# Performance work log

Hardware: AMD Instinct MI355X
Metric: run time of the kernel (lower is better)

The kernel has to match this reference:

```python
import jax, jax.numpy as jnp
import numpy as np

TOP_K = 2
B, S, H, I, E = 1, 2048, 1024, 4096, 8


def setup_inputs() -> dict:
    key = jax.random.key(0)
    k1, k2, k3, k4 = jax.random.split(key, 4)
    x = jax.random.normal(k1, (B, S, H), dtype=jnp.float32)
    gate_w = jax.random.normal(k2, (E, H), dtype=jnp.float32)
    w1 = jax.random.normal(k3, (E, I, H), dtype=jnp.float32)
    w2 = jax.random.normal(k4, (E, H, I), dtype=jnp.float32)
    return {"x": x, "gate_w": gate_w, "w1": w1, "w2": w2}


def reference(x, gate_w, w1, w2):
    b, s, h = x.shape
    xf = x.reshape(-1, h)                      # [T, H]
    T = xf.shape[0]
    logits = xf @ gate_w.T                     # [T, E]
    probs = jax.nn.softmax(logits, axis=-1)
    wts, idx = jax.lax.top_k(probs, TOP_K)     # [T, k]
    wts = wts / jnp.sum(wts, axis=-1, keepdims=True)
    # combine[t, e] = routing weight of expert e for token t (0 if not selected)
    combine = jnp.zeros((T, w1.shape[0]), dtype=x.dtype)
    combine = combine.at[jnp.arange(T)[:, None], idx].add(wts)
    # dense dispatch: every expert processes every token, masked/weighted by combine
    hid = jax.nn.silu(jnp.einsum('th,eih->tei', xf, w1))   # [T, E, I]
    y = jnp.einsum('tei,ehi->teh', hid, w2)                # [T, E, H]
    out = jnp.einsum('teh,te->th', y, combine)             # [T, H]
    return out.reshape(b, s, h)
```

## Files before the change

kernel.cpp:

```cpp
#include <hip/hip_runtime.h>
#include <stdint.h>

#define TT 2048
#define HH 1024
#define II 4096
#define EE 8
#define KS 4
#define KSPAN (II / KS)

typedef __attribute__((ext_vector_type(4))) float floatx4;
typedef __attribute__((ext_vector_type(8))) __bf16 bf16x8;

__device__ __forceinline__ unsigned short f2bf(float f) {
  union { float f; unsigned u; } v; v.f = f;
  return (unsigned short)((v.u + 0x7FFFu + ((v.u >> 16) & 1u)) >> 16);
}

__device__ __forceinline__ void async_ld16(const void* g, void* l) {
  __builtin_amdgcn_global_load_lds(
      (__attribute__((address_space(1))) void*)g,
      (__attribute__((address_space(3))) void*)l, 16, 0, 0);
}

#define CFENCE asm volatile("" ::: "memory")
#define WAIT_VM(n) asm volatile("s_waitcnt vmcnt(" #n ")" ::: "memory")
#define WAIT_LGKM0 asm volatile("s_waitcnt lgkmcnt(0)" ::: "memory")

__global__ __launch_bounds__(256) void k_gating(
    const float* __restrict__ x, const float* __restrict__ gw,
    unsigned short* __restrict__ xb, int* __restrict__ sel_e,
    float* __restrict__ sel_w, int* __restrict__ counts) {
  int t = blockIdx.x;
  int tid = threadIdx.x;
  floatx4 xv = ((const floatx4*)(x + (size_t)t * HH))[tid];
  ushort4 xo;
  xo.x = f2bf(xv.x); xo.y = f2bf(xv.y); xo.z = f2bf(xv.z); xo.w = f2bf(xv.w);
  ((ushort4*)(xb + (size_t)t * HH))[tid] = xo;

  float part[EE];
#pragma unroll
  for (int e = 0; e < EE; e++) {
    floatx4 g = ((const floatx4*)(gw + e * HH))[tid];
    part[e] = xv.x * g.x + xv.y * g.y + xv.z * g.z + xv.w * g.w;
  }
#pragma unroll
  for (int e = 0; e < EE; e++) {
    float v = part[e];
#pragma unroll
    for (int off = 32; off > 0; off >>= 1) v += __shfl_down(v, off, 64);
    part[e] = v;
  }
  __shared__ float red[4][EE];
  int wave = tid >> 6;
  if ((tid & 63) == 0) {
#pragma unroll
    for (int e = 0; e < EE; e++) red[wave][e] = part[e];
  }
  __syncthreads();
  if (tid == 0) {
    float lg[EE];
#pragma unroll
    for (int e = 0; e < EE; e++)
      lg[e] = red[0][e] + red[1][e] + red[2][e] + red[3][e];
    int e0 = 0;
#pragma unroll
    for (int e = 1; e < EE; e++) if (lg[e] > lg[e0]) e0 = e;
    int e1 = (e0 == 0) ? 1 : 0;
#pragma unroll
    for (int e = 0; e < EE; e++) if (e != e0 && lg[e] > lg[e1]) e1 = e;
    float w0 = 1.f / (1.f + expf(lg[e1] - lg[e0]));
    sel_e[t * 2] = e0; sel_e[t * 2 + 1] = e1;
    sel_w[t * 2] = w0; sel_w[t * 2 + 1] = 1.f - w0;
    atomicAdd(&counts[e0], 1);
    atomicAdd(&counts[e1], 1);
  }
}

__global__ __launch_bounds__(256) void k_fill(
    const int* __restrict__ counts, const int* __restrict__ sel_e,
    const float* __restrict__ sel_w, int* __restrict__ bases,
    int* __restrict__ row_token, float* __restrict__ row_w,
    int* __restrict__ inv_slot) {
  __shared__ int lb[EE];
  __shared__ int lc[EE];
  int tid = threadIdx.x;
  if (tid == 0) {
    int s = 0;
    for (int e = 0; e < EE; e++) { lb[e] = s; s += counts[e]; }
  }
  if (tid < EE) lc[tid] = 0;
  __syncthreads();
  for (int p = tid; p < TT * 2; p += 256) {
    int e = sel_e[p];
    int slot = lb[e] + atomicAdd(&lc[e], 1);
    row_token[slot] = p >> 1;
    row_w[slot] = sel_w[p];
    inv_slot[p] = slot;
  }
  __syncthreads();
  if (tid < EE) bases[tid] = lb[tid];
}

#define ISSUE_B(kt, ra, rb, rc, rd)                         \
  do {                                                      \
    ra = *(const floatx4*)(bp0 + (size_t)(kt) * 32);        \
    rb = *(const floatx4*)(bp0 + (size_t)(kt) * 32 + 4);    \
    rc = *(const floatx4*)(bp1 + (size_t)(kt) * 32);        \
    rd = *(const floatx4*)(bp1 + (size_t)(kt) * 32 + 4);    \
    CFENCE;                                                 \
  } while (0)

#define DMA_A(kt)                                           \
  do {                                                      \
    async_ld16(aS0 + (size_t)(kt) * 32, pA2 + ldsOff);      \
    async_ld16(aS1 + (size_t)(kt) * 32, pA2 + ldsOff + 2048); \
    CFENCE;                                                 \
  } while (0)

#define CVT_WR(ra, rb, rc, rd)                              \
  do {                                                      \
    bf16x8 wv0, wv1;                                        \
    _Pragma("unroll") for (int q = 0; q < 4; q++) {         \
      wv0[q] = (__bf16)ra[q]; wv0[q + 4] = (__bf16)rb[q];   \
      wv1[q] = (__bf16)rc[q]; wv1[q + 4] = (__bf16)rd[q];   \
    }                                                       \
    *(bf16x8*)(pB1 + ldsB) = wv0;                           \
    *(bf16x8*)(pB1 + ldsB + 2048) = wv1;                    \
  } while (0)

#define MFMA_STEP                                           \
  do {                                                      \
    bf16x8 af[4], bfr[4];                                   \
    _Pragma("unroll") for (int i = 0; i < 4; i++) {         \
      af[i]  = *(const bf16x8*)(pA0 + offA[i]);             \
      bfr[i] = *(const bf16x8*)(pB0 + offB[i]);             \
    }                                                       \
    _Pragma("unroll") for (int i = 0; i < 4; i++)           \
      _Pragma("unroll") for (int jj = 0; jj < 4; jj++)      \
        acc[i][jj] = __builtin_amdgcn_mfma_f32_16x16x32_bf16(af[i], bfr[jj], acc[i][jj], 0, 0, 0); \
  } while (0)

#define ROT3                                                \
  do {                                                      \
    unsigned short* t_ = pA0; pA0 = pA1; pA1 = pA2; pA2 = t_; \
    t_ = pB0; pB0 = pB1; pB1 = pB2; pB2 = t_;               \
  } while (0)

#define BAR  do { __builtin_amdgcn_s_barrier(); CFENCE; } while (0)

__global__ __launch_bounds__(256) void k_gemm1(
    const unsigned short* __restrict__ xb,
    const float* __restrict__ w1,
    unsigned short* __restrict__ hid,
    const int* __restrict__ counts, const int* __restrict__ bases,
    const int* __restrict__ row_token) {
  const int e = blockIdx.z;
  const int count = counts[e];
  const int m0 = blockIdx.y * 128;
  if (m0 >= count) return;
  const int n0 = blockIdx.x * 128;
  const int base = bases[e];

  __shared__ __align__(16) unsigned short Smem[6 * 4096];

  const int tid = threadIdx.x;
  const int lane = tid & 63;
  const int wave = tid >> 6;
  const int wm = (wave & 1) * 64;
  const int wn = (wave >> 1) * 64;
  const int quad = lane >> 4;
  const int l16 = lane & 15;

  const int rA0 = tid >> 2;
  const int swz = (tid & 3) ^ ((tid >> 3) & 3);
  const int ccA = swz * 8;
  const int ccB = (tid & 3) * 8;
  const int ldsOff = tid * 8;
  const int ldsB = rA0 * 32 + swz * 8;

  int g0 = m0 + rA0;      if (g0 > count - 1) g0 = count - 1;
  int g1 = m0 + rA0 + 64; if (g1 > count - 1) g1 = count - 1;
  const unsigned short* aS0 = xb + (size_t)row_token[base + g0] * HH + ccA;
  const unsigned short* aS1 = xb + (size_t)row_token[base + g1] * HH + ccA;
  const float* wp = w1 + (size_t)e * II * HH;
  const float* bp0 = wp + (size_t)(n0 + rA0) * HH + ccB;
  const float* bp1 = bp0 + (size_t)64 * HH;

  int offA[4], offB[4];
#pragma unroll
  for (int i = 0; i < 4; i++) {
    const int Ra = wm + i * 16 + l16;
    offA[i] = Ra * 32 + 8 * (quad ^ ((Ra >> 1) & 3));
    const int Rb = wn + i * 16 + l16;
    offB[i] = Rb * 32 + 8 * (quad ^ ((Rb >> 1) & 3));
  }

  const floatx4 fz = {0.f, 0.f, 0.f, 0.f};
  floatx4 acc[4][4];
#pragma unroll
  for (int i = 0; i < 4; i++)
#pragma unroll
    for (int j = 0; j < 4; j++) acc[i][j] = fz;

  unsigned short* pA0 = Smem;
  unsigned short* pA1 = Smem + 4096;
  unsigned short* pA2 = Smem + 8192;
  unsigned short* pB0 = Smem + 12288;
  unsigned short* pB1 = Smem + 16384;
  unsigned short* pB2 = Smem + 20480;

  floatx4 s0a, s0b, s0c, s0d;
  floatx4 s1a, s1b, s1c, s1d;

  ISSUE_B(0, s0a, s0b, s0c, s0d);
  { unsigned short* sv = pA2; pA2 = pA0; DMA_A(0); pA2 = sv; }
  ISSUE_B(1, s1a, s1b, s1c, s1d);
  { unsigned short* sv = pA2; pA2 = pA1; DMA_A(1); pA2 = sv; }
  WAIT_VM(6);
  { unsigned short* sv = pB1; pB1 = pB0; CVT_WR(s0a, s0b, s0c, s0d); pB1 = sv; }
  WAIT_LGKM0;
  BAR;

  for (int j = 0; j < 16; ++j) {
    const int k = 2 * j;
    if (j < 15) { ISSUE_B(k + 2, s0a, s0b, s0c, s0d); DMA_A(k + 2); }
    MFMA_STEP;
    if (j < 15) { WAIT_VM(6); } else { WAIT_VM(0); }
    CVT_WR(s1a, s1b, s1c, s1d);
    WAIT_LGKM0;
    BAR;
    ROT3;
    if (j < 15) { ISSUE_B(k + 3, s1a, s1b, s1c, s1d); DMA_A(k + 3); }
    MFMA_STEP;
    if (j < 15) {
      WAIT_VM(6);
      CVT_WR(s0a, s0b, s0c, s0d);
      WAIT_LGKM0;
      BAR;
      ROT3;
    }
  }
  __syncthreads();

  unsigned short* Sl = Smem + wave * (16 * 72);
#pragma unroll
  for (int i = 0; i < 4; i++) {
#pragma unroll
    for (int r = 0; r < 4; r++) {
      const int row16 = quad * 4 + r;
#pragma unroll
      for (int j = 0; j < 4; j++) {
        float z = acc[i][j][r];
        Sl[row16 * 72 + l16 + 16 * j] = f2bf(z / (1.f + __expf(-z)));
      }
    }
#pragma unroll
    for (int half = 0; half < 2; half++) {
      const int row16 = (lane >> 3) + 8 * half;
      const int m = wm + i * 16 + row16;
      if (m0 + m < count) {
        bf16x8 v = *(const bf16x8*)(Sl + row16 * 72 + (lane & 7) * 8);
        *(bf16x8*)(hid + (size_t)(base + m0 + m) * II + n0 + wn + (lane & 7) * 8) = v;
      }
    }
    __syncthreads();
  }
}

__global__ __launch_bounds__(256) void k_gemm2(
    const unsigned short* __restrict__ hid,
    const float* __restrict__ w2,
    float* __restrict__ yp,
    const int* __restrict__ counts, const int* __restrict__ bases) {
  const int e = blockIdx.z;
  const int count = counts[e];
  const int m0 = blockIdx.y * 128;
  if (m0 >= count) return;
  const int nt = blockIdx.x & 7;
  const int ks = blockIdx.x >> 3;
  const int n0 = nt * 128;
  const int base = bases[e];
  const int kbeg = ks * KSPAN;

  __shared__ __align__(16) unsigned short Smem2[6 * 4096];

  const int tid = threadIdx.x;
  const int lane = tid & 63;
  const int wave = tid >> 6;
  const int wm = (wave & 1) * 64;
  const int wn = (wave >> 1) * 64;
  const int quad = lane >> 4;
  const int l16 = lane & 15;

  const int rA0 = tid >> 2;
  const int swz = (tid & 3) ^ ((tid >> 3) & 3);
  const int ccA = swz * 8;
  const int ccB = (tid & 3) * 8;
  const int ldsOff = tid * 8;
  const int ldsB = rA0 * 32 + swz * 8;

  int g0 = m0 + rA0;      if (g0 > count - 1) g0 = count - 1;
  int g1 = m0 + rA0 + 64; if (g1 > count - 1) g1 = count - 1;
  const unsigned short* aS0 = hid + (size_t)(base + g0) * II + kbeg + ccA;
  const unsigned short* aS1 = hid + (size_t)(base + g1) * II + kbeg + ccA;
  const float* wp = w2 + (size_t)e * HH * II;
  const float* bp0 = wp + (size_t)(n0 + rA0) * II + kbeg + ccB;
  const float* bp1 = bp0 + (size_t)64 * II;

  int offA[4], offB[4];
#pragma unroll
  for (int i = 0; i < 4; i++) {
    const int Ra = wm + i * 16 + l16;
    offA[i] = Ra * 32 + 8 * (quad ^ ((Ra >> 1) & 3));
    const int Rb = wn + i * 16 + l16;
    offB[i] = Rb * 32 + 8 * (quad ^ ((Rb >> 1) & 3));
  }

  const floatx4 fz = {0.f, 0.f, 0.f, 0.f};
  floatx4 acc[4][4];
#pragma unroll
  for (int i = 0; i < 4; i++)
#pragma unroll
    for (int j = 0; j < 4; j++) acc[i][j] = fz;

  unsigned short* pA0 = Smem2;
  unsigned short* pA1 = Smem2 + 4096;
  unsigned short* pA2 = Smem2 + 8192;
  unsigned short* pB0 = Smem2 + 12288;
  unsigned short* pB1 = Smem2 + 16384;
  unsigned short* pB2 = Smem2 + 20480;

  floatx4 s0a, s0b, s0c, s0d;
  floatx4 s1a, s1b, s1c, s1d;

  ISSUE_B(0, s0a, s0b, s0c, s0d);
  { unsigned short* sv = pA2; pA2 = pA0; DMA_A(0); pA2 = sv; }
  ISSUE_B(1, s1a, s1b, s1c, s1d);
  { unsigned short* sv = pA2; pA2 = pA1; DMA_A(1); pA2 = sv; }
  WAIT_VM(6);
  { unsigned short* sv = pB1; pB1 = pB0; CVT_WR(s0a, s0b, s0c, s0d); pB1 = sv; }
  WAIT_LGKM0;
  BAR;

  for (int j = 0; j < 16; ++j) {
    const int k = 2 * j;
    if (j < 15) { ISSUE_B(k + 2, s0a, s0b, s0c, s0d); DMA_A(k + 2); }
    MFMA_STEP;
    if (j < 15) { WAIT_VM(6); } else { WAIT_VM(0); }
    CVT_WR(s1a, s1b, s1c, s1d);
    WAIT_LGKM0;
    BAR;
    ROT3;
    if (j < 15) { ISSUE_B(k + 3, s1a, s1b, s1c, s1d); DMA_A(k + 3); }
    MFMA_STEP;
    if (j < 15) {
      WAIT_VM(6);
      CVT_WR(s0a, s0b, s0c, s0d);
      WAIT_LGKM0;
      BAR;
      ROT3;
    }
  }

#pragma unroll
  for (int i = 0; i < 4; i++) {
#pragma unroll
    for (int r = 0; r < 4; r++) {
      const int m = wm + i * 16 + quad * 4 + r;
      if (m0 + m < count) {
        float* op = yp + ((size_t)ks * (TT * 2) + base + m0 + m) * HH + n0 + wn + l16;
#pragma unroll
        for (int j = 0; j < 4; j++) op[j * 16] = acc[i][j][r];
      }
    }
  }
}

__global__ __launch_bounds__(256) void k_combine(
    const float* __restrict__ yp, const int* __restrict__ inv_slot,
    const float* __restrict__ sel_w, float* __restrict__ out) {
  const int t = blockIdx.x;
  const int tid = threadIdx.x;
  const int s0 = inv_slot[2 * t];
  const int s1 = inv_slot[2 * t + 1];
  const float w0 = sel_w[2 * t];
  const float w1 = sel_w[2 * t + 1];
  floatx4 a = {0.f, 0.f, 0.f, 0.f};
  floatx4 b = {0.f, 0.f, 0.f, 0.f};
#pragma unroll
  for (int ks = 0; ks < KS; ks++) {
    a += ((const floatx4*)(yp + ((size_t)ks * (TT * 2) + s0) * HH))[tid];
    b += ((const floatx4*)(yp + ((size_t)ks * (TT * 2) + s1) * HH))[tid];
  }
  floatx4 v = w0 * a + w1 * b;
  ((floatx4*)(out + (size_t)t * HH))[tid] = v;
}

extern "C" void kernel_launch(void* const* d_in, const int* in_sizes, int n_in,
                              void* d_out, int out_size, void* d_ws, size_t ws_size,
                              hipStream_t stream) {
  const float* x  = (const float*)d_in[0];
  const float* gw = (const float*)d_in[1];
  const float* w1 = (const float*)d_in[2];
  const float* w2 = (const float*)d_in[3];
  float* out = (float*)d_out;

  char* ws = (char*)d_ws;
  size_t off = 0;
  auto take = [&](size_t n) -> char* {
    char* p = ws + off;
    off += (n + 255) & ~(size_t)255;
    return p;
  };
  unsigned short* xb  = (unsigned short*)take((size_t)TT * HH * 2);
  unsigned short* hid = (unsigned short*)take((size_t)TT * 2 * II * 2);
  float* yp = (float*)take((size_t)KS * (TT * 2) * HH * 4);
  int*   counts    = (int*)take(EE * 4);
  int*   bases     = (int*)take(EE * 4);
  int*   row_token = (int*)take((size_t)TT * 2 * 4);
  float* row_w     = (float*)take((size_t)TT * 2 * 4);
  int*   sel_e     = (int*)take((size_t)TT * 2 * 4);
  float* sel_w     = (float*)take((size_t)TT * 2 * 4);
  int*   inv_slot  = (int*)take((size_t)TT * 2 * 4);
  if (off > ws_size) return;

  hipMemsetAsync(counts, 0, EE * 4, stream);

  k_gating<<<TT, 256, 0, stream>>>(x, gw, xb, sel_e, sel_w, counts);
  k_fill<<<1, 256, 0, stream>>>(counts, sel_e, sel_w, bases, row_token, row_w, inv_slot);
  k_gemm1<<<dim3(II / 128, 16, EE), 256, 0, stream>>>(xb, w1, hid, counts, bases, row_token);
  k_gemm2<<<dim3(8 * KS, 16, EE), 256, 0, stream>>>(hid, w2, yp, counts, bases);
  k_combine<<<TT, 256, 0, stream>>>(yp, inv_slot, sel_w, out);
}
```

Baseline: 483.9 us.

## Enlarge MoE GEMM M-tile to 256 rows with a double-buffered pipeline

Both expert GEMMs now use 256-row M tiles, with each wave computing 128x64 outputs, so the fp32 weights of each expert are streamed and converted for half as many M tiles. The three-stage rotating LDS pipeline, which carried two register sets of B loads, becomes a two-stage ping-pong that waits for all outstanding loads every iteration. The per-iteration barrier in the gemm1 epilogue is also dropped, since each wave uses its own staging region. In exchange the kernels hold twice as many accumulators, use fewer blocks, and overlap load latency with compute less.

```diff
diff --git a/kernel.cpp b/kernel.cpp
--- a/kernel.cpp
+++ b/kernel.cpp
@@ -7,6 +7,8 @@
 #define EE 8
 #define KS 4
 #define KSPAN (II / KS)
+#define BM 256
+#define BN 128
 
 typedef __attribute__((ext_vector_type(4))) float floatx4;
 typedef __attribute__((ext_vector_type(8))) __bf16 bf16x8;
@@ -101,52 +103,48 @@
   if (tid < EE) bases[tid] = lb[tid];
 }
 
-#define ISSUE_B(kt, ra, rb, rc, rd)                         \
+#define ISSUE_B(kt)                                         \
   do {                                                      \
-    ra = *(const floatx4*)(bp0 + (size_t)(kt) * 32);        \
-    rb = *(const floatx4*)(bp0 + (size_t)(kt) * 32 + 4);    \
-    rc = *(const floatx4*)(bp1 + (size_t)(kt) * 32);        \
-    rd = *(const floatx4*)(bp1 + (size_t)(kt) * 32 + 4);    \
+    ba = *(const floatx4*)(bp0 + (size_t)(kt) * 32);        \
+    bb = *(const floatx4*)(bp0 + (size_t)(kt) * 32 + 4);    \
+    bc = *(const floatx4*)(bp1 + (size_t)(kt) * 32);        \
+    bd = *(const floatx4*)(bp1 + (size_t)(kt) * 32 + 4);    \
     CFENCE;                                                 \
   } while (0)
 
-#define DMA_A(kt)                                           \
+#define DMA_A(kt, pA)                                       \
   do {                                                      \
-    async_ld16(aS0 + (size_t)(kt) * 32, pA2 + ldsOff);      \
-    async_ld16(aS1 + (size_t)(kt) * 32, pA2 + ldsOff + 2048); \
+    async_ld16(aS0 + (size_t)(kt) * 32, (pA) + ldsOff);     \
+    async_ld16(aS1 + (size_t)(kt) * 32, (pA) + ldsOff + 2048); \
+    async_ld16(aS2 + (size_t)(kt) * 32, (pA) + ldsOff + 4096); \
+    async_ld16(aS3 + (size_t)(kt) * 32, (pA) + ldsOff + 6144); \
     CFENCE;                                                 \
   } while (0)
 
-#define CVT_WR(ra, rb, rc, rd)                              \
+#define CVT_WR(pB)                                          \
   do {                                                      \
     bf16x8 wv0, wv1;                                        \
     _Pragma("unroll") for (int q = 0; q < 4; q++) {         \
-      wv0[q] = (__bf16)ra[q]; wv0[q + 4] = (__bf16)rb[q];   \
-      wv1[q] = (__bf16)rc[q]; wv1[q + 4] = (__bf16)rd[q];   \
+      wv0[q] = (__bf16)ba[q]; wv0[q + 4] = (__bf16)bb[q];   \
+      wv1[q] = (__bf16)bc[q]; wv1[q + 4] = (__bf16)bd[q];   \
     }                                                       \
-    *(bf16x8*)(pB1 + ldsB) = wv0;                           \
-    *(bf16x8*)(pB1 + ldsB + 2048) = wv1;                    \
+    *(bf16x8*)((pB) + ldsB) = wv0;                          \
+    *(bf16x8*)((pB) + ldsB + 2048) = wv1;                   \
   } while (0)
 
-#define MFMA_STEP                                           \
+#define MFMA_STEP(pAc, pBc)                                 \
   do {                                                      \
-    bf16x8 af[4], bfr[4];                                   \
-    _Pragma("unroll") for (int i = 0; i < 4; i++) {         \
-      af[i]  = *(const bf16x8*)(pA0 + offA[i]);             \
-      bfr[i] = *(const bf16x8*)(pB0 + offB[i]);             \
+    bf16x8 bfr[4];                                          \
+    _Pragma("unroll") for (int j = 0; j < 4; j++)           \
+      bfr[j] = *(const bf16x8*)((pBc) + offB[j]);           \
+    _Pragma("unroll") for (int i = 0; i < 8; i++) {         \
+      bf16x8 af = *(const bf16x8*)((pAc) + offA[i]);        \
+      _Pragma("unroll") for (int j = 0; j < 4; j++)         \
+        acc[i][j] = __builtin_amdgcn_mfma_f32_16x16x32_bf16(af, bfr[j], acc[i][j], 0, 0, 0); \
     }                                                       \
-    _Pragma("unroll") for (int i = 0; i < 4; i++)           \
-      _Pragma("unroll") for (int jj = 0; jj < 4; jj++)      \
-        acc[i][jj] = __builtin_amdgcn_mfma_f32_16x16x32_bf16(af[i], bfr[jj], acc[i][jj], 0, 0, 0); \
   } while (0)
 
-#define ROT3                                                \
-  do {                                                      \
-    unsigned short* t_ = pA0; pA0 = pA1; pA1 = pA2; pA2 = t_; \
-    t_ = pB0; pB0 = pB1; pB1 = pB2; pB2 = t_;               \
-  } while (0)
-
-#define BAR  do { __builtin_amdgcn_s_barrier(); CFENCE; } while (0)
+#define BAR do { __builtin_amdgcn_s_barrier(); CFENCE; } while (0)
 
 __global__ __launch_bounds__(256) void k_gemm1(
     const unsigned short* __restrict__ xb,
@@ -156,17 +154,21 @@
     const int* __restrict__ row_token) {
   const int e = blockIdx.z;
   const int count = counts[e];
-  const int m0 = blockIdx.y * 128;
+  const int m0 = blockIdx.y * BM;
   if (m0 >= count) return;
-  const int n0 = blockIdx.x * 128;
+  const int n0 = blockIdx.x * BN;
   const int base = bases[e];
 
-  __shared__ __align__(16) unsigned short Smem[6 * 4096];
+  __shared__ __align__(16) unsigned short Smem[24576];
+  unsigned short* const A0 = Smem;
+  unsigned short* const A1 = Smem + 8192;
+  unsigned short* const B0 = Smem + 16384;
+  unsigned short* const B1 = Smem + 20480;
 
   const int tid = threadIdx.x;
   const int lane = tid & 63;
   const int wave = tid >> 6;
-  const int wm = (wave & 1) * 64;
+  const int wm2 = (wave & 1) * 128;
   const int wn = (wave >> 1) * 64;
   const int quad = lane >> 4;
   const int l16 = lane & 15;
@@ -178,73 +180,66 @@
   const int ldsOff = tid * 8;
   const int ldsB = rA0 * 32 + swz * 8;
 
-  int g0 = m0 + rA0;      if (g0 > count - 1) g0 = count - 1;
-  int g1 = m0 + rA0 + 64; if (g1 > count - 1) g1 = count - 1;
+  int g0 = m0 + rA0;       if (g0 > count - 1) g0 = count - 1;
+  int g1 = m0 + rA0 + 64;  if (g1 > count - 1) g1 = count - 1;
+  int g2 = m0 + rA0 + 128; if (g2 > count - 1) g2 = count - 1;
+  int g3 = m0 + rA0 + 192; if (g3 > count - 1) g3 = count - 1;
   const unsigned short* aS0 = xb + (size_t)row_token[base + g0] * HH + ccA;
   const unsigned short* aS1 = xb + (size_t)row_token[base + g1] * HH + ccA;
+  const unsigned short* aS2 = xb + (size_t)row_token[base + g2] * HH + ccA;
+  const unsigned short* aS3 = xb + (size_t)row_token[base + g3] * HH + ccA;
   const float* wp = w1 + (size_t)e * II * HH;
   const float* bp0 = wp + (size_t)(n0 + rA0) * HH + ccB;
   const float* bp1 = bp0 + (size_t)64 * HH;
 
-  int offA[4], offB[4];
-#pragma unroll
-  for (int i = 0; i < 4; i++) {
-    const int Ra = wm + i * 16 + l16;
+  int offA[8], offB[4];
+#pragma unroll
+  for (int i = 0; i < 8; i++) {
+    const int Ra = wm2 + i * 16 + l16;
     offA[i] = Ra * 32 + 8 * (quad ^ ((Ra >> 1) & 3));
-    const int Rb = wn + i * 16 + l16;
-    offB[i] = Rb * 32 + 8 * (quad ^ ((Rb >> 1) & 3));
+  }
+#pragma unroll
+  for (int j = 0; j < 4; j++) {
+    const int Rb = wn + j * 16 + l16;
+    offB[j] = Rb * 32 + 8 * (quad ^ ((Rb >> 1) & 3));
   }
 
   const floatx4 fz = {0.f, 0.f, 0.f, 0.f};
-  floatx4 acc[4][4];
-#pragma unroll
-  for (int i = 0; i < 4; i++)
+  floatx4 acc[8][4];
+#pragma unroll
+  for (int i = 0; i < 8; i++)
 #pragma unroll
     for (int j = 0; j < 4; j++) acc[i][j] = fz;
 
-  unsigned short* pA0 = Smem;
-  unsigned short* pA1 = Smem + 4096;
-  unsigned short* pA2 = Smem + 8192;
-  unsigned short* pB0 = Smem + 12288;
-  unsigned short* pB1 = Smem + 16384;
-  unsigned short* pB2 = Smem + 20480;
-
-  floatx4 s0a, s0b, s0c, s0d;
-  floatx4 s1a, s1b, s1c, s1d;
-
-  ISSUE_B(0, s0a, s0b, s0c, s0d);
-  { unsigned short* sv = pA2; pA2 = pA0; DMA_A(0); pA2 = sv; }
-  ISSUE_B(1, s1a, s1b, s1c, s1d);
-  { unsigned short* sv = pA2; pA2 = pA1; DMA_A(1); pA2 = sv; }
-  WAIT_VM(6);
-  { unsigned short* sv = pB1; pB1 = pB0; CVT_WR(s0a, s0b, s0c, s0d); pB1 = sv; }
+  floatx4 ba, bb, bc, bd;
+
+  ISSUE_B(0);
+  DMA_A(0, A0);
+  WAIT_VM(4);
+  CVT_WR(B0);
+  WAIT_VM(0);
   WAIT_LGKM0;
   BAR;
 
-  for (int j = 0; j < 16; ++j) {
-    const int k = 2 * j;
-    if (j < 15) { ISSUE_B(k + 2, s0a, s0b, s0c, s0d); DMA_A(k + 2); }
-    MFMA_STEP;
-    if (j < 15) { WAIT_VM(6); } else { WAIT_VM(0); }
-    CVT_WR(s1a, s1b, s1c, s1d);
+  unsigned short* pAc = A0; unsigned short* pAn = A1;
+  unsigned short* pBc = B0; unsigned short* pBn = B1;
+
+  for (int kt = 0; kt < HH / 32; ++kt) {
+    const bool has = (kt < HH / 32 - 1);
+    if (has) { ISSUE_B(kt + 1); DMA_A(kt + 1, pAn); }
+    MFMA_STEP(pAc, pBc);
+    if (has) { WAIT_VM(4); CVT_WR(pBn); }
+    WAIT_VM(0);
     WAIT_LGKM0;
     BAR;
-    ROT3;
-    if (j < 15) { ISSUE_B(k + 3, s1a, s1b, s1c, s1d); DMA_A(k + 3); }
-    MFMA_STEP;
-    if (j < 15) {
-      WAIT_VM(6);
-      CVT_WR(s0a, s0b, s0c, s0d);
-      WAIT_LGKM0;
-      BAR;
-      ROT3;
-    }
+    { unsigned short* t = pAc; pAc = pAn; pAn = t; }
+    { unsigned short* t = pBc; pBc = pBn; pBn = t; }
   }
   __syncthreads();
 
   unsigned short* Sl = Smem + wave * (16 * 72);
 #pragma unroll
-  for (int i = 0; i < 4; i++) {
+  for (int i = 0; i < 8; i++) {
 #pragma unroll
     for (int r = 0; r < 4; r++) {
       const int row16 = quad * 4 + r;
@@ -257,13 +252,12 @@
 #pragma unroll
     for (int half = 0; half < 2; half++) {
       const int row16 = (lane >> 3) + 8 * half;
-      const int m = wm + i * 16 + row16;
+      const int m = wm2 + i * 16 + row16;
       if (m0 + m < count) {
         bf16x8 v = *(const bf16x8*)(Sl + row16 * 72 + (lane & 7) * 8);
         *(bf16x8*)(hid + (size_t)(base + m0 + m) * II + n0 + wn + (lane & 7) * 8) = v;
       }
     }
-    __syncthreads();
   }
 }
 
@@ -274,20 +268,24 @@
     const int* __restrict__ counts, const int* __restrict__ bases) {
   const int e = blockIdx.z;
   const int count = counts[e];
-  const int m0 = blockIdx.y * 128;
+  const int m0 = blockIdx.y * BM;
   if (m0 >= count) return;
   const int nt = blockIdx.x & 7;
   const int ks = blockIdx.x >> 3;
-  const int n0 = nt * 128;
+  const int n0 = nt * BN;
   const int base = bases[e];
   const int kbeg = ks * KSPAN;
 
-  __shared__ __align__(16) unsigned short Smem2[6 * 4096];
+  __shared__ __align__(16) unsigned short Smem2[24576];
+  unsigned short* const A0 = Smem2;
+  unsigned short* const A1 = Smem2 + 8192;
+  unsigned short* const B0 = Smem2 + 16384;
+  unsigned short* const B1 = Smem2 + 20480;
 
   const int tid = threadIdx.x;
   const int lane = tid & 63;
   const int wave = tid >> 6;
-  const int wm = (wave & 1) * 64;
+  const int wm2 = (wave & 1) * 128;
   const int wn = (wave >> 1) * 64;
   const int quad = lane >> 4;
   const int l16 = lane & 15;
@@ -299,74 +297,67 @@
   const int ldsOff = tid * 8;
   const int ldsB = rA0 * 32 + swz * 8;
 
-  int g0 = m0 + rA0;      if (g0 > count - 1) g0 = count - 1;
-  int g1 = m0 + rA0 + 64; if (g1 > count - 1) g1 = count - 1;
+  int g0 = m0 + rA0;       if (g0 > count - 1) g0 = count - 1;
+  int g1 = m0 + rA0 + 64;  if (g1 > count - 1) g1 = count - 1;
+  int g2 = m0 + rA0 + 128; if (g2 > count - 1) g2 = count - 1;
+  int g3 = m0 + rA0 + 192; if (g3 > count - 1) g3 = count - 1;
   const unsigned short* aS0 = hid + (size_t)(base + g0) * II + kbeg + ccA;
   const unsigned short* aS1 = hid + (size_t)(base + g1) * II + kbeg + ccA;
+  const unsigned short* aS2 = hid + (size_t)(base + g2) * II + kbeg + ccA;
+  const unsigned short* aS3 = hid + (size_t)(base + g3) * II + kbeg + ccA;
   const float* wp = w2 + (size_t)e * HH * II;
   const float* bp0 = wp + (size_t)(n0 + rA0) * II + kbeg + ccB;
   const float* bp1 = bp0 + (size_t)64 * II;
 
-  int offA[4], offB[4];
-#pragma unroll
-  for (int i = 0; i < 4; i++) {
-    const int Ra = wm + i * 16 + l16;
+  int offA[8], offB[4];
+#pragma unroll
+  for (int i = 0; i < 8; i++) {
+    const int Ra = wm2 + i * 16 + l16;
     offA[i] = Ra * 32 + 8 * (quad ^ ((Ra >> 1) & 3));
-    const int Rb = wn + i * 16 + l16;
-    offB[i] = Rb * 32 + 8 * (quad ^ ((Rb >> 1) & 3));
+  }
+#pragma unroll
+  for (int j = 0; j < 4; j++) {
+    const int Rb = wn + j * 16 + l16;
+    offB[j] = Rb * 32 + 8 * (quad ^ ((Rb >> 1) & 3));
   }
 
   const floatx4 fz = {0.f, 0.f, 0.f, 0.f};
-  floatx4 acc[4][4];
-#pragma unroll
-  for (int i = 0; i < 4; i++)
+  floatx4 acc[8][4];
+#pragma unroll
+  for (int i = 0; i < 8; i++)
 #pragma unroll
     for (int j = 0; j < 4; j++) acc[i][j] = fz;
 
-  unsigned short* pA0 = Smem2;
-  unsigned short* pA1 = Smem2 + 4096;
-  unsigned short* pA2 = Smem2 + 8192;
-  unsigned short* pB0 = Smem2 + 12288;
-  unsigned short* pB1 = Smem2 + 16384;
-  unsigned short* pB2 = Smem2 + 20480;
-
-  floatx4 s0a, s0b, s0c, s0d;
-  floatx4 s1a, s1b, s1c, s1d;
-
-  ISSUE_B(0, s0a, s0b, s0c, s0d);
-  { unsigned short* sv = pA2; pA2 = pA0; DMA_A(0); pA2 = sv; }
-  ISSUE_B(1, s1a, s1b, s1c, s1d);
-  { unsigned short* sv = pA2; pA2 = pA1; DMA_A(1); pA2 = sv; }
-  WAIT_VM(6);
-  { unsigned short* sv = pB1; pB1 = pB0; CVT_WR(s0a, s0b, s0c, s0d); pB1 = sv; }
+  floatx4 ba, bb, bc, bd;
+
+  ISSUE_B(0);
+  DMA_A(0, A0);
+  WAIT_VM(4);
+  CVT_WR(B0);
+  WAIT_VM(0);
   WAIT_LGKM0;
   BAR;
 
-  for (int j = 0; j < 16; ++j) {
-    const int k = 2 * j;
-    if (j < 15) { ISSUE_B(k + 2, s0a, s0b, s0c, s0d); DMA_A(k + 2); }
-    MFMA_STEP;
-    if (j < 15) { WAIT_VM(6); } else { WAIT_VM(0); }
-    CVT_WR(s1a, s1b, s1c, s1d);
+  unsigned short* pAc = A0; unsigned short* pAn = A1;
+  unsigned short* pBc = B0; unsigned short* pBn = B1;
+
+  for (int kt = 0; kt < KSPAN / 32; ++kt) {
+    const bool has = (kt < KSPAN / 32 - 1);
+    if (has) { ISSUE_B(kt + 1); DMA_A(kt + 1, pAn); }
+    MFMA_STEP(pAc, pBc);
+    if (has) { WAIT_VM(4); CVT_WR(pBn); }
+    WAIT_VM(0);
     WAIT_LGKM0;
     BAR;
-    ROT3;
-    if (j < 15) { ISSUE_B(k + 3, s1a, s1b, s1c, s1d); DMA_A(k + 3); }
-    MFMA_STEP;
-    if (j < 15) {
-      WAIT_VM(6);
-      CVT_WR(s0a, s0b, s0c, s0d);
-      WAIT_LGKM0;
-      BAR;
-      ROT3;
-    }
-  }
-
-#pragma unroll
-  for (int i = 0; i < 4; i++) {
+    { unsigned short* t = pAc; pAc = pAn; pAn = t; }
+    { unsigned short* t = pBc; pBc = pBn; pBn = t; }
+  }
+
+#pragma unroll
+  for (int i = 0; i < 8; i++) {
 #pragma unroll
     for (int r = 0; r < 4; r++) {
-      const int m = wm + i * 16 + quad * 4 + r;
+      const int m = wm2 + i * 16 + quad * 4 + r;
       if (m0 + m < count) {
         float* op = yp + ((size_t)ks * (TT * 2) + base + m0 + m) * HH + n0 + wn + l16;
 #pragma unroll
@@ -428,7 +419,7 @@
 
   k_gating<<<TT, 256, 0, stream>>>(x, gw, xb, sel_e, sel_w, counts);
   k_fill<<<1, 256, 0, stream>>>(counts, sel_e, sel_w, bases, row_token, row_w, inv_slot);
-  k_gemm1<<<dim3(II / 128, 16, EE), 256, 0, stream>>>(xb, w1, hid, counts, bases, row_token);
-  k_gemm2<<<dim3(8 * KS, 16, EE), 256, 0, stream>>>(hid, w2, yp, counts, bases);
+  k_gemm1<<<dim3(II / BN, 8, EE), 256, 0, stream>>>(xb, w1, hid, counts, bases, row_token);
+  k_gemm2<<<dim3(8 * KS, 8, EE), 256, 0, stream>>>(hid, w2, yp, counts, bases);
   k_combine<<<TT, 256, 0, stream>>>(yp, inv_slot, sel_w, out);
 }
```

Measured after the change: 505.9 us. +4.6%, slower.
